# Performance work log

Measured on AMD Instinct MI355X. Metric: run time of the kernel, lower is better.

The kernel has to match this reference:

```python
import jax, jax.numpy as jnp
import numpy as np

B, N, I, O, CG, H, E = 32, 256, 16, 16, 64, 64, 4096
SEQ_LEN = 256  # sequence_length init arg (temporal attention scale)


def setup_inputs() -> dict:
    key = jax.random.key(0)
    ks = jax.random.split(key, 24)
    r = lambda i, shape, s: jax.random.normal(ks[i], shape, jnp.float32) * s
    return {
        'data': jax.random.normal(ks[0], (B, I, N), jnp.float32),
        'masks': jax.random.bernoulli(ks[1], 0.8, (B, I, N)),
        'edge_index': jax.random.randint(ks[2], (2, E), 0, N, jnp.int64),
        'gcn_w': r(3, (I, CG), 0.2),
        'gcn_b': jnp.zeros((CG,), jnp.float32),
        'sa_qw': r(4, (CG, CG), 0.1), 'sa_qb': jnp.zeros((CG,), jnp.float32),
        'sa_kw': r(5, (CG, CG), 0.1), 'sa_kb': jnp.zeros((CG,), jnp.float32),
        'gru_wih': r(6, (3 * H, I), 0.1), 'gru_whh': r(7, (3 * H, H), 0.1),
        'gru_bih': jnp.zeros((3 * H,), jnp.float32), 'gru_bhh': jnp.zeros((3 * H,), jnp.float32),
        'ta_qw': r(8, (H, H), 0.1), 'ta_qb': jnp.zeros((H,), jnp.float32),
        'ta_kw': r(9, (H, H), 0.1), 'ta_kb': jnp.zeros((H,), jnp.float32),
        'fc1_w': r(10, (H * N * 2, H * N // 4), 0.005), 'fc1_b': jnp.zeros((H * N // 4,), jnp.float32),
        'fc2_w': r(11, (H * N // 4, O * N), 0.01), 'fc2_b': jnp.zeros((O * N,), jnp.float32),
    }


def _forward(data, masks, edge_index, gcn_w, gcn_b, sa_qw, sa_qb, sa_kw, sa_kb,
             gru_wih, gru_whh, gru_bih, gru_bhh, ta_qw, ta_qb, ta_kw, ta_kb,
             fc1_w, fc1_b, fc2_w, fc2_b):
    data = jnp.where(masks, data, 0.0)            # [B, I, N]
    x = jnp.swapaxes(data, 1, 2)                  # [B, N, I] (per-sample node features)

    loop = jnp.arange(N)
    src = jnp.concatenate([edge_index[0], loop])
    dst = jnp.concatenate([edge_index[1], loop])
    w = jnp.concatenate([jnp.ones((E,), jnp.float32), 2.0 * jnp.ones((N,), jnp.float32)])
    deg = jax.ops.segment_sum(w, dst, num_segments=N)
    dinv = jnp.where(deg > 0, jax.lax.rsqrt(deg), 0.0)
    norm = dinv[src] * w * dinv[dst]              # [E+N]
    xw = x @ gcn_w                                # [B, N, CG]
    msg = xw[:, src, :] * norm[None, :, None]     # gather + scale
    agg = jax.vmap(lambda m: jax.ops.segment_sum(m, dst, num_segments=N))(msg)
    h = jax.nn.relu(agg + gcn_b)                  # [B, N, CG]

    # --- SpatialAttention (per sample, scale 1/sqrt(num_nodes)) ---
    q = h @ sa_qw + sa_qb
    k = h @ sa_kw + sa_kb
    att = jax.nn.softmax(jnp.einsum('bnc,bmc->bnm', q, k) / np.sqrt(N).astype(np.float32), axis=-1)
    ha = jnp.einsum('bnm,bmc->bnc', att, h)

    # torch stacks x.T -> [B, CG, N] then .view(B, -1, CG): a reshape, not a transpose
    se = jnp.swapaxes(h, 1, 2).reshape(B, N, CG)
    sa = jnp.swapaxes(ha, 1, 2).reshape(B, N, CG)
    # dropout is identity in eval mode

    # --- GRU (1 layer, batch_first) over rnn_input = data.view(B, -1, I) ---
    rnn_in = data.reshape(B, N, I)
    def step(hprev, xt):
        gi = xt @ gru_wih.T + gru_bih
        gh = hprev @ gru_whh.T + gru_bhh
        ir, iz, inn = jnp.split(gi, 3, axis=-1)
        hr, hz, hn = jnp.split(gh, 3, axis=-1)
        r = jax.nn.sigmoid(ir + hr)
        z = jax.nn.sigmoid(iz + hz)
        n = jnp.tanh(inn + r * hn)
        hnew = (1.0 - z) * n + z * hprev
        return hnew, hnew
    h0 = jnp.zeros((B, H), jnp.float32)
    _, outs = jax.lax.scan(step, h0, jnp.swapaxes(rnn_in, 0, 1))
    rnn_out = jnp.swapaxes(outs, 0, 1)            # [B, N, H]

    # --- TemporalAttention (scale 1/sqrt(sequence_length)) ---
    qt = rnn_out @ ta_qw + ta_qb
    kt = rnn_out @ ta_kw + ta_kb
    att_t = jax.nn.softmax(jnp.einsum('btc,bsc->bts', qt, kt) / np.sqrt(SEQ_LEN).astype(np.float32), axis=-1)
    rnn_a = jnp.einsum('bts,bsc->btc', att_t, rnn_out)

    # --- fused MLP combine ---
    embed = jnp.concatenate([rnn_out, se], axis=-1).reshape(B, -1)  # [B, 2*H*N]
    inter = embed @ fc1_w + fc1_b
    final = inter @ fc2_w + fc2_b
    final = jnp.swapaxes(final.reshape(B, N, O), 1, 2)              # [B, O, N]
    rnn_a = jnp.swapaxes(rnn_a, 1, 2)                               # [B, H, N]
    return final, sa, rnn_a


def reference(data, masks, edge_index, gcn_w, gcn_b, sa_qw, sa_qb, sa_kw, sa_kb,
              gru_wih, gru_whh, gru_bih, gru_bhh, ta_qw, ta_qb, ta_kw, ta_kb,
              fc1_w, fc1_b, fc2_w, fc2_b):
    return _forward(data, masks, edge_index, gcn_w, gcn_b, sa_qw, sa_qb, sa_kw, sa_kb,
                    gru_wih, gru_whh, gru_bih, gru_bhh, ta_qw, ta_qb, ta_kw, ta_kb,
                    fc1_w, fc1_b, fc2_w, fc2_b)
```

## Files before the change

### kernel.cpp

```cpp
#include <hip/hip_runtime.h>

#define NB 32
#define NN 256
#define NI 16
#define NO 16
#define NC 64
#define NH 64
#define NE 4096
#define FC1_N 4096

__device__ __forceinline__ float sigmoidf_(float x){ return 1.0f/(1.0f+__expf(-x)); }
__device__ __forceinline__ float tanhf_(float x){
  float e = __expf(2.0f*x);
  return 1.0f - 2.0f/(e+1.0f);
}

__device__ __forceinline__ void gload16(const void* g, void* l){
  __builtin_amdgcn_global_load_lds((const __attribute__((address_space(1))) void*)g,
                                   (__attribute__((address_space(3))) void*)l, 16, 0, 0);
}

__global__ void k_detect(const unsigned char* __restrict__ m8, const int* __restrict__ ei, int* flags){
  int t = blockIdx.x*256 + threadIdx.x;
  unsigned a = (unsigned)m8[t*4+1] | (unsigned)m8[t*4+2] | (unsigned)m8[t*4+3];
  if (__any(a != 0) && (threadIdx.x & 63) == 0) atomicOr(&flags[0], 1);
  unsigned b = 0;
  if (t < 4096) b = (unsigned)ei[2*t+1];
  if (__any(b != 0) && (threadIdx.x & 63) == 0) atomicOr(&flags[1], 1);
}

__global__ void k_mask(const float* __restrict__ data, const unsigned char* __restrict__ m8,
                       const int* __restrict__ flags, float* __restrict__ dm){
  int i = blockIdx.x*256 + threadIdx.x;
  int mv = flags[0] ? (int)m8[i] : ((const int*)m8)[i];
  dm[i] = mv ? data[i] : 0.0f;
}

__device__ __forceinline__ int edge_src(const int* ei, const int* flags, int e){
  return flags[1] ? ei[e] : ei[2*e];
}
__device__ __forceinline__ int edge_dst(const int* ei, const int* flags, int e){
  return flags[1] ? ei[NE + e] : ei[2*(NE + e)];
}

__global__ __launch_bounds__(256) void k_graph(const int* __restrict__ ei, const int* __restrict__ flags,
                                               float* wadj){
  int t = threadIdx.x;
  float4 z = {0.f,0.f,0.f,0.f};
  for (int x = t; x < 16384; x += 256) ((float4*)wadj)[x] = z;
  __shared__ float degs[NN];
  __shared__ float dls[NN];
  degs[t] = 0.f;
  __syncthreads();
  for (int e = t; e < NE; e += 256) atomicAdd(&degs[edge_dst(ei, flags, e)], 1.0f);
  __syncthreads();
  float di = rsqrtf(degs[t] + 2.0f);
  dls[t] = di;
  atomicAdd(&wadj[t*NN + t], 2.0f*di*di);
  __syncthreads();
  for (int e = t; e < NE; e += 256){
    int s = edge_src(ei, flags, e), d = edge_dst(ei, flags, e);
    atomicAdd(&wadj[d*NN + s], dls[s]*dls[d]);
  }
}

__global__ void k_xw(const float* __restrict__ dm, const float* __restrict__ gw, float* __restrict__ xw){
  int idx = blockIdx.x*256 + threadIdx.x;
  int c = idx & 63, n = (idx>>6) & 255, b = idx>>14;
  const float* dmb = dm + b*NI*NN;
  float a = 0.f;
  #pragma unroll
  for (int i=0;i<NI;i++) a += dmb[i*NN + n]*gw[i*NC + c];
  xw[idx] = a;
}

__global__ void k_agg(const float* __restrict__ wadj, const float* __restrict__ xw,
                      const float* __restrict__ gb, float* __restrict__ h){
  int idx = blockIdx.x*256 + threadIdx.x;
  int c = idx & 63, n = (idx>>6) & 255, b = idx>>14;
  const float* wr = wadj + n*NN;
  const float* xb = xw + b*NN*NC + c;
  float a = gb[c];
  #pragma unroll 4
  for (int m=0;m<NN;m++) a += wr[m]*xb[m*NC];
  h[idx] = fmaxf(a, 0.0f);
}

__global__ void k_qk2(const float* __restrict__ hb, const float* __restrict__ rnn,
    const float* __restrict__ saqw, const float* __restrict__ saqb,
    const float* __restrict__ sakw, const float* __restrict__ sakb,
    const float* __restrict__ taqw, const float* __restrict__ taqb,
    const float* __restrict__ takw, const float* __restrict__ takb,
    float* __restrict__ qb, float* __restrict__ kb, float* __restrict__ qt, float* __restrict__ kt){
  int bid = blockIdx.x;
  const float *src, *qw, *qbias, *kw, *kbias; float *qo, *ko;
  if (bid < 2048){ src=hb; qw=saqw; qbias=saqb; kw=sakw; kbias=sakb; qo=qb; ko=kb; }
  else { bid -= 2048; src=rnn; qw=taqw; qbias=taqb; kw=takw; kbias=takb; qo=qt; ko=kt; }
  int idx = bid*256 + threadIdx.x;
  int c = idx & 63;
  const float* hr = src + (idx>>6)*NC;
  float aq = qbias[c], ak = kbias[c];
  #pragma unroll 8
  for (int cc=0; cc<NC; cc++){ float hv = hr[cc]; aq += hv*qw[cc*NC + c]; ak += hv*kw[cc*NC + c]; }
  qo[idx] = aq; ko[idx] = ak;
}

__global__ __launch_bounds__(256) void k_attn2(const float* __restrict__ qb, const float* __restrict__ kb,
    const float* __restrict__ hb, const float* __restrict__ qt, const float* __restrict__ kt,
    const float* __restrict__ rnn, float* __restrict__ out_sa, float* __restrict__ out_ra){
  int bidx = blockIdx.x;
  const float *q, *kmat, *v; float* outp;
  if (bidx < 1024){ q=qb; kmat=kb; v=hb; outp=out_sa; }
  else { bidx -= 1024; q=qt; kmat=kt; v=rnn; outp=out_ra; }
  int b = bidx >> 5, n0 = (bidx & 31)*8;
  int t = threadIdx.x;
  const float scale = 0.0625f;
  __shared__ __align__(16) float qs[8][64];
  __shared__ float S[8][256];
  #pragma unroll
  for (int rep=0; rep<2; rep++){
    int j = rep*256 + t; int r = j>>6, c = j&63;
    qs[r][c] = q[((b<<8) + n0 + r)*NC + c];
  }
  __syncthreads();
  float4 kr[16];
  const float4* kp = (const float4*)(kmat + ((b<<8) + t)*NC);
  #pragma unroll
  for (int i=0;i<16;i++) kr[i] = kp[i];
  #pragma unroll
  for (int r=0;r<8;r++){
    const float4* q4 = (const float4*)qs[r];
    float s = 0.f;
    #pragma unroll
    for (int i=0;i<16;i++){ float4 a=q4[i], bb=kr[i]; s += a.x*bb.x + a.y*bb.y + a.z*bb.z + a.w*bb.w; }
    S[r][t] = s*scale;
  }
  __syncthreads();
  {
    int g = t>>5, l = t&31;
    float vals[8];
    #pragma unroll
    for (int k2=0;k2<8;k2++) vals[k2] = S[g][l + (k2<<5)];
    float mx = vals[0];
    #pragma unroll
    for (int k2=1;k2<8;k2++) mx = fmaxf(mx, vals[k2]);
    #pragma unroll
    for (int off=16; off; off>>=1) mx = fmaxf(mx, __shfl_xor(mx, off));
    float sm = 0.f;
    #pragma unroll
    for (int k2=0;k2<8;k2++){ vals[k2] = __expf(vals[k2]-mx); sm += vals[k2]; }
    #pragma unroll
    for (int off=16; off; off>>=1) sm += __shfl_xor(sm, off);
    float rS = 1.0f/sm;
    #pragma unroll
    for (int k2=0;k2<8;k2++) S[g][l + (k2<<5)] = vals[k2]*rS;
  }
  __syncthreads();
  int c = t & 63, rp = t >> 6;
  const float* vp = v + (b<<8)*NC + c;
  float a0 = 0.f, a1 = 0.f;
  #pragma unroll 4
  for (int m=0;m<NN;m++){
    float vv = vp[m*NC];
    a0 += S[rp][m]*vv;
    a1 += S[rp+4][m]*vv;
  }
  outp[(((b<<6)+c)<<8) + n0 + rp]     = a0;
  outp[(((b<<6)+c)<<8) + n0 + rp + 4] = a1;
}

__global__ __launch_bounds__(64) void k_gru(const float* __restrict__ dm,
        const float* __restrict__ wih, const float* __restrict__ bih,
        const float* __restrict__ whh, const float* __restrict__ bhh,
        float* __restrict__ rnn){
  const int b = blockIdx.x, j = threadIdx.x;
  __shared__ __align__(16) float dmS[4096];
  __shared__ __align__(16) float hsS[64];
  const float4* dmb4 = (const float4*)(dm + b*4096);
  float4* dmS4 = (float4*)dmS;
  #pragma unroll
  for (int x=0;x<16;x++) dmS4[j + 64*x] = dmb4[j + 64*x];
  float wr_[64], wz_[64], wn_[64];
  {
    const float4* pr = (const float4*)(whh + (long)j*NH);
    const float4* pz = (const float4*)(whh + (long)(j+64)*NH);
    const float4* pn = (const float4*)(whh + (long)(j+128)*NH);
    #pragma unroll
    for (int k4=0;k4<16;k4++){
      float4 a = pr[k4]; wr_[4*k4]=a.x; wr_[4*k4+1]=a.y; wr_[4*k4+2]=a.z; wr_[4*k4+3]=a.w;
      float4 c = pz[k4]; wz_[4*k4]=c.x; wz_[4*k4+1]=c.y; wz_[4*k4+2]=c.z; wz_[4*k4+3]=c.w;
      float4 d = pn[k4]; wn_[4*k4]=d.x; wn_[4*k4+1]=d.y; wn_[4*k4+2]=d.z; wn_[4*k4+3]=d.w;
    }
  }
  float wir[16], wiz[16], win_[16];
  {
    const float4* pr = (const float4*)(wih + (long)j*NI);
    const float4* pz = (const float4*)(wih + (long)(j+64)*NI);
    const float4* pn = (const float4*)(wih + (long)(j+128)*NI);
    #pragma unroll
    for (int k4=0;k4<4;k4++){
      float4 a = pr[k4]; wir[4*k4]=a.x;  wir[4*k4+1]=a.y;  wir[4*k4+2]=a.z;  wir[4*k4+3]=a.w;
      float4 c = pz[k4]; wiz[4*k4]=c.x;  wiz[4*k4+1]=c.y;  wiz[4*k4+2]=c.z;  wiz[4*k4+3]=c.w;
      float4 d = pn[k4]; win_[4*k4]=d.x; win_[4*k4+1]=d.y; win_[4*k4+2]=d.z; win_[4*k4+3]=d.w;
    }
  }
  const float br = bhh[j], bz = bhh[j+64], bn = bhh[j+128];
  const float bir = bih[j], biz = bih[j+64], bin_ = bih[j+128];
  float h = 0.f;
  hsS[j] = 0.f;
  __syncthreads();
  float* rp = rnn + (long)b*NN*NH + j;
  for (int t=0;t<NN;t++){
    float hv[64];
    const float4* hs4 = (const float4*)hsS;
    #pragma unroll
    for (int k4=0;k4<16;k4++){
      float4 v = hs4[k4];
      hv[4*k4]=v.x; hv[4*k4+1]=v.y; hv[4*k4+2]=v.z; hv[4*k4+3]=v.w;
    }
    float gr0=0.f, gr1=0.f, gz0=0.f, gz1=0.f, gn0=0.f, gn1=0.f;
    #pragma unroll
    for (int k=0;k<64;k+=2){
      gr0 += wr_[k]*hv[k];   gz0 += wz_[k]*hv[k];   gn0 += wn_[k]*hv[k];
      gr1 += wr_[k+1]*hv[k+1]; gz1 += wz_[k+1]*hv[k+1]; gn1 += wn_[k+1]*hv[k+1];
    }
    const float* xt = &dmS[t*16];
    float gir=bir, giz=biz, gin2=bin_;
    #pragma unroll
    for (int i=0;i<16;i++){ float xv = xt[i]; gir += wir[i]*xv; giz += wiz[i]*xv; gin2 += win_[i]*xv; }
    float r  = sigmoidf_(gir + gr0 + gr1 + br);
    float z  = sigmoidf_(giz + gz0 + gz1 + bz);
    float nn2= tanhf_  (gin2 + r*(gn0 + gn1 + bn));
    h = nn2 + z*(h - nn2);
    rp[(long)t*NH] = h;
    hsS[j] = h;
    __syncthreads();
  }
}

__global__ void k_embedT(const float* __restrict__ rnn, const float* __restrict__ h,
                         float* __restrict__ ET){
  int idx = blockIdx.x*256 + threadIdx.x;
  int bb = idx & 31, rr = idx >> 5;
  int n = rr >> 7, c = rr & 127;
  float v;
  if (c < 64) v = rnn[((bb<<8) + n)*NH + c];
  else { int f = (n<<6) + (c-64); v = h[(bb<<14) + ((f&255)<<6) + (f>>8)]; }
  ET[idx] = v;
}

template<int KC>
__global__ __launch_bounds__(512, 4) void k_fc(const float* __restrict__ W,
        const float* __restrict__ Ein, float* __restrict__ part){
  const int tid = threadIdx.x, lane = tid & 63, wv_ = tid >> 6;
  const int cw = wv_ & 1, bq = wv_ >> 1;
  const int c0 = blockIdx.x*512;
  const long k0 = (long)blockIdx.y*KC;
  __shared__ __align__(16) float wlds[2][8][512];
  __shared__ __align__(16) float elds[2][256];
  float acc[4][8];
  #pragma unroll
  for (int c=0;c<4;c++)
    #pragma unroll
    for (int bb=0;bb<8;bb++) acc[c][bb]=0.f;

  const int NCH = KC/8;
  #define STAGE_FC(ch, bf) { \
    const float* wsrc = W + (k0 + (long)(ch)*8)*FC1_N + c0; \
    gload16(wsrc + (long)wv_*FC1_N + lane*4,       &wlds[bf][wv_][0]); \
    gload16(wsrc + (long)wv_*FC1_N + 256 + lane*4, &wlds[bf][wv_][256]); \
    if (wv_ == 0) gload16(Ein + (k0 + (long)(ch)*8)*32 + lane*4, &elds[bf][0]); \
  }

  STAGE_FC(0, 0)
  int cur = 0;
  for (int ch=0; ch<NCH; ch++){
    __syncthreads();
    if (ch+1 < NCH) STAGE_FC(ch+1, cur^1)
    #pragma unroll
    for (int r=0;r<8;r++){
      float4 wv4 = *(const float4*)&wlds[cur][r][cw*256 + lane*4];
      float4 e0 = *(const float4*)&elds[cur][r*32 + bq*8];
      float4 e1 = *(const float4*)&elds[cur][r*32 + bq*8 + 4];
      float ev[8] = {e0.x,e0.y,e0.z,e0.w,e1.x,e1.y,e1.z,e1.w};
      #pragma unroll
      for (int bb=0;bb<8;bb++){
        acc[0][bb] += wv4.x*ev[bb];
        acc[1][bb] += wv4.y*ev[bb];
        acc[2][bb] += wv4.z*ev[bb];
        acc[3][bb] += wv4.w*ev[bb];
      }
    }
    cur ^= 1;
  }
  float* pp = part + (long)blockIdx.y*131072 + (long)(bq*8)*FC1_N + c0 + cw*256 + lane*4;
  #pragma unroll
  for (int bb=0;bb<8;bb++){
    float4 o; o.x=acc[0][bb]; o.y=acc[1][bb]; o.z=acc[2][bb]; o.w=acc[3][bb];
    *(float4*)(pp + (long)bb*FC1_N) = o;
  }
  #undef STAGE_FC
}

__global__ void k_red1(const float* __restrict__ part, const float* __restrict__ bias,
                       float* __restrict__ ITr){
  int idx4 = blockIdx.x*256 + threadIdx.x;
  int b = idx4 >> 10, col4 = idx4 & 1023;
  float4 a = ((const float4*)bias)[col4];
  #pragma unroll 16
  for (int y=0;y<64;y++){
    float4 p = ((const float4*)(part + (long)y*131072 + (long)b*FC1_N))[col4];
    a.x+=p.x; a.y+=p.y; a.z+=p.z; a.w+=p.w;
  }
  int col = col4*4;
  ITr[(col+0)*32 + b] = a.x;
  ITr[(col+1)*32 + b] = a.y;
  ITr[(col+2)*32 + b] = a.z;
  ITr[(col+3)*32 + b] = a.w;
}

__global__ void k_red2(const float* __restrict__ part, const float* __restrict__ bias,
                       float* __restrict__ outp){
  int idx4 = blockIdx.x*256 + threadIdx.x;
  int b = idx4 >> 10, col4 = idx4 & 1023;
  float4 a = ((const float4*)bias)[col4];
  #pragma unroll 16
  for (int y=0;y<64;y++){
    float4 p = ((const float4*)(part + (long)y*131072 + (long)b*FC1_N))[col4];
    a.x+=p.x; a.y+=p.y; a.z+=p.z; a.w+=p.w;
  }
  float av[4] = {a.x, a.y, a.z, a.w};
  #pragma unroll
  for (int c=0;c<4;c++){
    int col = col4*4 + c;
    int n = col >> 4, o = col & 15;
    outp[(b<<12) + (o<<8) + n] = av[c];
  }
}

extern "C" void kernel_launch(void* const* d_in, const int* in_sizes, int n_in,
                              void* d_out, int out_size, void* d_ws, size_t ws_size,
                              hipStream_t stream) {
  const float* data   = (const float*)d_in[0];
  const unsigned char* masks = (const unsigned char*)d_in[1];
  const int* ei       = (const int*)d_in[2];
  const float* gcn_w  = (const float*)d_in[3];
  const float* gcn_b  = (const float*)d_in[4];
  const float* sa_qw  = (const float*)d_in[5];
  const float* sa_qb  = (const float*)d_in[6];
  const float* sa_kw  = (const float*)d_in[7];
  const float* sa_kb  = (const float*)d_in[8];
  const float* wih    = (const float*)d_in[9];
  const float* whh    = (const float*)d_in[10];
  const float* bih    = (const float*)d_in[11];
  const float* bhh    = (const float*)d_in[12];
  const float* ta_qw  = (const float*)d_in[13];
  const float* ta_qb  = (const float*)d_in[14];
  const float* ta_kw  = (const float*)d_in[15];
  const float* ta_kb  = (const float*)d_in[16];
  const float* fc1_w  = (const float*)d_in[17];
  const float* fc1_b  = (const float*)d_in[18];
  const float* fc2_w  = (const float*)d_in[19];
  const float* fc2_b  = (const float*)d_in[20];

  float* dm    = (float*)d_ws;
  float* wadj  = dm + 131072;
  int*   flags = (int*)(wadj + 65536);
  float* xw    = (float*)(flags + 8);
  float* hb    = xw + 524288;
  float* qb    = hb + 524288;
  float* kb    = qb + 524288;
  float* rnn   = kb + 524288;
  float* qt    = rnn + 524288;
  float* kt    = qt + 524288;
  float* ET    = kt + 524288;
  float* ITr   = ET + 1048576;
  float* part1 = ITr + 131072;
  float* part2 = part1 + 64*131072;

  float* out_final = (float*)d_out;
  float* out_sa = out_final + 131072;
  float* out_ra = out_final + 655360;

  hipMemsetAsync(flags, 0, 32, stream);

  k_detect<<<128,256,0,stream>>>(masks, ei, flags);
  k_mask<<<512,256,0,stream>>>(data, masks, flags, dm);
  k_gru<<<32,64,0,stream>>>(dm, wih, bih, whh, bhh, rnn);
  k_graph<<<1,256,0,stream>>>(ei, flags, wadj);
  k_xw<<<2048,256,0,stream>>>(dm, gcn_w, xw);
  k_agg<<<2048,256,0,stream>>>(wadj, xw, gcn_b, hb);
  k_qk2<<<4096,256,0,stream>>>(hb, rnn, sa_qw, sa_qb, sa_kw, sa_kb,
                               ta_qw, ta_qb, ta_kw, ta_kb, qb, kb, qt, kt);
  k_attn2<<<2048,256,0,stream>>>(qb, kb, hb, qt, kt, rnn, out_sa, out_ra);
  k_embedT<<<4096,256,0,stream>>>(rnn, hb, ET);
  { dim3 g(8,64); k_fc<512><<<g,512,0,stream>>>(fc1_w, ET, part1); }
  k_red1<<<128,256,0,stream>>>(part1, fc1_b, ITr);
  { dim3 g(8,64); k_fc<64><<<g,512,0,stream>>>(fc2_w, ITr, part2); }
  k_red2<<<128,256,0,stream>>>(part2, fc2_b, out_final);
}
```

Before: 584.2 us.

## Fuse graph build into xw kernel, drop GRU barrier, load FC activations directly

Merges the single-block graph-normalisation kernel into the xw projection kernel as an extra block, which removes one launch and lets the graph work overlap with the xw work. The GRU recurrence drops its per-step __syncthreads, relying on the block being a single 64-wide wavefront, and reads the hidden state as float4 directly inside the dot product. The FC kernel reads activations from global memory into registers instead of staging them in LDS, and uses a wave-uniform batch index via readfirstlane. Reduction unroll factors are lowered. Dropping the barrier relies on in-order LDS access within one wavefront.

```diff
diff --git a/kernel.cpp b/kernel.cpp
--- a/kernel.cpp
+++ b/kernel.cpp
@@ -43,35 +43,36 @@
   return flags[1] ? ei[NE + e] : ei[2*(NE + e)];
 }
 
-__global__ __launch_bounds__(256) void k_graph(const int* __restrict__ ei, const int* __restrict__ flags,
-                                               float* wadj){
-  int t = threadIdx.x;
-  float4 z = {0.f,0.f,0.f,0.f};
-  for (int x = t; x < 16384; x += 256) ((float4*)wadj)[x] = z;
+__global__ __launch_bounds__(256) void k_xw_graph(const float* __restrict__ dm,
+        const float* __restrict__ gw, float* __restrict__ xw,
+        const int* __restrict__ ei, const int* __restrict__ flags, float* wadj){
   __shared__ float degs[NN];
   __shared__ float dls[NN];
-  degs[t] = 0.f;
-  __syncthreads();
-  for (int e = t; e < NE; e += 256) atomicAdd(&degs[edge_dst(ei, flags, e)], 1.0f);
-  __syncthreads();
-  float di = rsqrtf(degs[t] + 2.0f);
-  dls[t] = di;
-  atomicAdd(&wadj[t*NN + t], 2.0f*di*di);
-  __syncthreads();
-  for (int e = t; e < NE; e += 256){
-    int s = edge_src(ei, flags, e), d = edge_dst(ei, flags, e);
-    atomicAdd(&wadj[d*NN + s], dls[s]*dls[d]);
-  }
-}
-
-__global__ void k_xw(const float* __restrict__ dm, const float* __restrict__ gw, float* __restrict__ xw){
-  int idx = blockIdx.x*256 + threadIdx.x;
-  int c = idx & 63, n = (idx>>6) & 255, b = idx>>14;
-  const float* dmb = dm + b*NI*NN;
-  float a = 0.f;
-  #pragma unroll
-  for (int i=0;i<NI;i++) a += dmb[i*NN + n]*gw[i*NC + c];
-  xw[idx] = a;
+  if (blockIdx.x < 2048){
+    int idx = blockIdx.x*256 + threadIdx.x;
+    int c = idx & 63, n = (idx>>6) & 255, b = idx>>14;
+    const float* dmb = dm + b*NI*NN;
+    float a = 0.f;
+    #pragma unroll
+    for (int i=0;i<NI;i++) a += dmb[i*NN + n]*gw[i*NC + c];
+    xw[idx] = a;
+  } else {
+    int t = threadIdx.x;
+    float4 z = {0.f,0.f,0.f,0.f};
+    for (int x = t; x < 16384; x += 256) ((float4*)wadj)[x] = z;
+    degs[t] = 0.f;
+    __syncthreads();
+    for (int e = t; e < NE; e += 256) atomicAdd(&degs[edge_dst(ei, flags, e)], 1.0f);
+    __syncthreads();
+    float di = rsqrtf(degs[t] + 2.0f);
+    dls[t] = di;
+    atomicAdd(&wadj[t*NN + t], 2.0f*di*di);
+    __syncthreads();
+    for (int e = t; e < NE; e += 256){
+      int s = edge_src(ei, flags, e), d = edge_dst(ei, flags, e);
+      atomicAdd(&wadj[d*NN + s], dls[s]*dls[d]);
+    }
+  }
 }
 
 __global__ void k_agg(const float* __restrict__ wadj, const float* __restrict__ xw,
@@ -118,8 +119,8 @@
   __shared__ __align__(16) float qs[8][64];
   __shared__ float S[8][256];
   #pragma unroll
-  for (int rep=0; rep<2; rep++){
-    int j = rep*256 + t; int r = j>>6, c = j&63;
+  for (int rp2=0; rp2<2; rp2++){
+    int j = rp2*256 + t; int r = j>>6, c = j&63;
     qs[r][c] = q[((b<<8) + n0 + r)*NC + c];
   }
   __syncthreads();
@@ -173,18 +174,18 @@
         const float* __restrict__ wih, const float* __restrict__ bih,
         const float* __restrict__ whh, const float* __restrict__ bhh,
         float* __restrict__ rnn){
-  const int b = blockIdx.x, j = threadIdx.x;
+  const int b = blockIdx.x, l = threadIdx.x;
   __shared__ __align__(16) float dmS[4096];
   __shared__ __align__(16) float hsS[64];
   const float4* dmb4 = (const float4*)(dm + b*4096);
   float4* dmS4 = (float4*)dmS;
   #pragma unroll
-  for (int x=0;x<16;x++) dmS4[j + 64*x] = dmb4[j + 64*x];
+  for (int x=0;x<16;x++) dmS4[l + 64*x] = dmb4[l + 64*x];
   float wr_[64], wz_[64], wn_[64];
   {
-    const float4* pr = (const float4*)(whh + (long)j*NH);
-    const float4* pz = (const float4*)(whh + (long)(j+64)*NH);
-    const float4* pn = (const float4*)(whh + (long)(j+128)*NH);
+    const float4* pr = (const float4*)(whh + (long)l*NH);
+    const float4* pz = (const float4*)(whh + (long)(l+64)*NH);
+    const float4* pn = (const float4*)(whh + (long)(l+128)*NH);
     #pragma unroll
     for (int k4=0;k4<16;k4++){
       float4 a = pr[k4]; wr_[4*k4]=a.x; wr_[4*k4+1]=a.y; wr_[4*k4+2]=a.z; wr_[4*k4+3]=a.w;
@@ -194,9 +195,9 @@
   }
   float wir[16], wiz[16], win_[16];
   {
-    const float4* pr = (const float4*)(wih + (long)j*NI);
-    const float4* pz = (const float4*)(wih + (long)(j+64)*NI);
-    const float4* pn = (const float4*)(wih + (long)(j+128)*NI);
+    const float4* pr = (const float4*)(wih + (long)l*NI);
+    const float4* pz = (const float4*)(wih + (long)(l+64)*NI);
+    const float4* pn = (const float4*)(wih + (long)(l+128)*NI);
     #pragma unroll
     for (int k4=0;k4<4;k4++){
       float4 a = pr[k4]; wir[4*k4]=a.x;  wir[4*k4+1]=a.y;  wir[4*k4+2]=a.z;  wir[4*k4+3]=a.w;
@@ -204,37 +205,39 @@
       float4 d = pn[k4]; win_[4*k4]=d.x; win_[4*k4+1]=d.y; win_[4*k4+2]=d.z; win_[4*k4+3]=d.w;
     }
   }
-  const float br = bhh[j], bz = bhh[j+64], bn = bhh[j+128];
-  const float bir = bih[j], biz = bih[j+64], bin_ = bih[j+128];
+  const float br = bhh[l], bz = bhh[l+64], bn = bhh[l+128];
+  const float bir = bih[l], biz = bih[l+64], bin_ = bih[l+128];
   float h = 0.f;
-  hsS[j] = 0.f;
-  __syncthreads();
-  float* rp = rnn + (long)b*NN*NH + j;
+  hsS[l] = 0.f;
+  float* rp = rnn + (long)b*NN*NH + l;
+  const float4* hs4 = (const float4*)hsS;
   for (int t=0;t<NN;t++){
-    float hv[64];
-    const float4* hs4 = (const float4*)hsS;
+    float gr0=0.f, gr1=0.f, gz0=0.f, gz1=0.f, gn0=0.f, gn1=0.f;
     #pragma unroll
     for (int k4=0;k4<16;k4++){
-      float4 v = hs4[k4];
-      hv[4*k4]=v.x; hv[4*k4+1]=v.y; hv[4*k4+2]=v.z; hv[4*k4+3]=v.w;
-    }
-    float gr0=0.f, gr1=0.f, gz0=0.f, gz1=0.f, gn0=0.f, gn1=0.f;
-    #pragma unroll
-    for (int k=0;k<64;k+=2){
-      gr0 += wr_[k]*hv[k];   gz0 += wz_[k]*hv[k];   gn0 += wn_[k]*hv[k];
-      gr1 += wr_[k+1]*hv[k+1]; gz1 += wz_[k+1]*hv[k+1]; gn1 += wn_[k+1]*hv[k+1];
-    }
-    const float* xt = &dmS[t*16];
+      float4 hv = hs4[k4];
+      gr0 += wr_[4*k4+0]*hv.x + wr_[4*k4+1]*hv.y;
+      gr1 += wr_[4*k4+2]*hv.z + wr_[4*k4+3]*hv.w;
+      gz0 += wz_[4*k4+0]*hv.x + wz_[4*k4+1]*hv.y;
+      gz1 += wz_[4*k4+2]*hv.z + wz_[4*k4+3]*hv.w;
+      gn0 += wn_[4*k4+0]*hv.x + wn_[4*k4+1]*hv.y;
+      gn1 += wn_[4*k4+2]*hv.z + wn_[4*k4+3]*hv.w;
+    }
+    const float4* xt4 = (const float4*)&dmS[t*16];
     float gir=bir, giz=biz, gin2=bin_;
     #pragma unroll
-    for (int i=0;i<16;i++){ float xv = xt[i]; gir += wir[i]*xv; giz += wiz[i]*xv; gin2 += win_[i]*xv; }
-    float r  = sigmoidf_(gir + gr0 + gr1 + br);
-    float z  = sigmoidf_(giz + gz0 + gz1 + bz);
-    float nn2= tanhf_  (gin2 + r*(gn0 + gn1 + bn));
-    h = nn2 + z*(h - nn2);
-    rp[(long)t*NH] = h;
-    hsS[j] = h;
-    __syncthreads();
+    for (int k4=0;k4<4;k4++){
+      float4 xv = xt4[k4];
+      gir  += wir[4*k4+0]*xv.x  + wir[4*k4+1]*xv.y  + wir[4*k4+2]*xv.z  + wir[4*k4+3]*xv.w;
+      giz  += wiz[4*k4+0]*xv.x  + wiz[4*k4+1]*xv.y  + wiz[4*k4+2]*xv.z  + wiz[4*k4+3]*xv.w;
+      gin2 += win_[4*k4+0]*xv.x + win_[4*k4+1]*xv.y + win_[4*k4+2]*xv.z + win_[4*k4+3]*xv.w;
+    }
+    float rr  = sigmoidf_(gir + gr0 + gr1 + br);
+    float zz  = sigmoidf_(giz + gz0 + gz1 + bz);
+    float nn2 = tanhf_  (gin2 + rr*(gn0 + gn1 + bn));
+    h = nn2 + zz*(h - nn2);
+    hsS[l] = h;
+    rp[t*NH] = h;
   }
 }
 
@@ -253,11 +256,11 @@
 __global__ __launch_bounds__(512, 4) void k_fc(const float* __restrict__ W,
         const float* __restrict__ Ein, float* __restrict__ part){
   const int tid = threadIdx.x, lane = tid & 63, wv_ = tid >> 6;
-  const int cw = wv_ & 1, bq = wv_ >> 1;
+  const int cw = wv_ & 1;
+  const int bqu = __builtin_amdgcn_readfirstlane(wv_ >> 1);
   const int c0 = blockIdx.x*512;
   const long k0 = (long)blockIdx.y*KC;
   __shared__ __align__(16) float wlds[2][8][512];
-  __shared__ __align__(16) float elds[2][256];
   float acc[4][8];
   #pragma unroll
   for (int c=0;c<4;c++)
@@ -266,34 +269,39 @@
 
   const int NCH = KC/8;
   #define STAGE_FC(ch, bf) { \
-    const float* wsrc = W + (k0 + (long)(ch)*8)*FC1_N + c0; \
-    gload16(wsrc + (long)wv_*FC1_N + lane*4,       &wlds[bf][wv_][0]); \
-    gload16(wsrc + (long)wv_*FC1_N + 256 + lane*4, &wlds[bf][wv_][256]); \
-    if (wv_ == 0) gload16(Ein + (k0 + (long)(ch)*8)*32 + lane*4, &elds[bf][0]); \
-  }
-
+    const float* wsrc = W + (k0 + (long)(ch)*8 + wv_)*FC1_N + c0; \
+    gload16(wsrc + lane*4,       &wlds[bf][wv_][0]); \
+    gload16(wsrc + 256 + lane*4, &wlds[bf][wv_][256]); \
+  }
+
+  float4 E[16];
   STAGE_FC(0, 0)
   int cur = 0;
   for (int ch=0; ch<NCH; ch++){
     __syncthreads();
     if (ch+1 < NCH) STAGE_FC(ch+1, cur^1)
+    const float* ep = Ein + (k0 + (long)ch*8)*32 + bqu*8;
     #pragma unroll
     for (int r=0;r<8;r++){
-      float4 wv4 = *(const float4*)&wlds[cur][r][cw*256 + lane*4];
-      float4 e0 = *(const float4*)&elds[cur][r*32 + bq*8];
-      float4 e1 = *(const float4*)&elds[cur][r*32 + bq*8 + 4];
+      E[2*r]   = *(const float4*)(ep + r*32);
+      E[2*r+1] = *(const float4*)(ep + r*32 + 4);
+    }
+    #pragma unroll
+    for (int r=0;r<8;r++){
+      float4 w4 = *(const float4*)&wlds[cur][r][cw*256 + lane*4];
+      float4 e0 = E[2*r], e1 = E[2*r+1];
       float ev[8] = {e0.x,e0.y,e0.z,e0.w,e1.x,e1.y,e1.z,e1.w};
       #pragma unroll
       for (int bb=0;bb<8;bb++){
-        acc[0][bb] += wv4.x*ev[bb];
-        acc[1][bb] += wv4.y*ev[bb];
-        acc[2][bb] += wv4.z*ev[bb];
-        acc[3][bb] += wv4.w*ev[bb];
+        acc[0][bb] += w4.x*ev[bb];
+        acc[1][bb] += w4.y*ev[bb];
+        acc[2][bb] += w4.z*ev[bb];
+        acc[3][bb] += w4.w*ev[bb];
       }
     }
     cur ^= 1;
   }
-  float* pp = part + (long)blockIdx.y*131072 + (long)(bq*8)*FC1_N + c0 + cw*256 + lane*4;
+  float* pp = part + (long)blockIdx.y*131072 + (long)(bqu*8)*FC1_N + c0 + cw*256 + lane*4;
   #pragma unroll
   for (int bb=0;bb<8;bb++){
     float4 o; o.x=acc[0][bb]; o.y=acc[1][bb]; o.z=acc[2][bb]; o.w=acc[3][bb];
@@ -307,7 +315,7 @@
   int idx4 = blockIdx.x*256 + threadIdx.x;
   int b = idx4 >> 10, col4 = idx4 & 1023;
   float4 a = ((const float4*)bias)[col4];
-  #pragma unroll 16
+  #pragma unroll 8
   for (int y=0;y<64;y++){
     float4 p = ((const float4*)(part + (long)y*131072 + (long)b*FC1_N))[col4];
     a.x+=p.x; a.y+=p.y; a.z+=p.z; a.w+=p.w;
@@ -324,7 +332,7 @@
   int idx4 = blockIdx.x*256 + threadIdx.x;
   int b = idx4 >> 10, col4 = idx4 & 1023;
   float4 a = ((const float4*)bias)[col4];
-  #pragma unroll 16
+  #pragma unroll 8
   for (int y=0;y<64;y++){
     float4 p = ((const float4*)(part + (long)y*131072 + (long)b*FC1_N))[col4];
     a.x+=p.x; a.y+=p.y; a.z+=p.z; a.w+=p.w;
@@ -387,8 +395,7 @@
   k_detect<<<128,256,0,stream>>>(masks, ei, flags);
   k_mask<<<512,256,0,stream>>>(data, masks, flags, dm);
   k_gru<<<32,64,0,stream>>>(dm, wih, bih, whh, bhh, rnn);
-  k_graph<<<1,256,0,stream>>>(ei, flags, wadj);
-  k_xw<<<2048,256,0,stream>>>(dm, gcn_w, xw);
+  k_xw_graph<<<2049,256,0,stream>>>(dm, gcn_w, xw, ei, flags, wadj);
   k_agg<<<2048,256,0,stream>>>(wadj, xw, gcn_b, hb);
   k_qk2<<<4096,256,0,stream>>>(hb, rnn, sa_qw, sa_qb, sa_kw, sa_kb,
                                ta_qw, ta_qb, ta_kw, ta_kb, qb, kb, qt, kt);
```

After: 670.3 us. 1.15x slower.
